# Kernel tuning notes

Measured on AMD Instinct MI355X. Metric: run time of the kernel, lower is better.

## Reference

```python
import jax, jax.numpy as jnp
import numpy as np

B = 524288
H = 64  # hidden_dim
D = 1   # input_dim


def setup_inputs() -> dict:
    key = jax.random.key(0)
    ks = jax.random.split(key, 16)
    s = 0.05
    inp = {
        "gradients": jax.random.normal(ks[0], (B, D), jnp.float32),
        "parameters": jax.random.normal(ks[1], (B, D), jnp.float32),
        "momentum": jax.random.normal(ks[2], (B, D), jnp.float32),
        "h0": jax.random.normal(ks[3], (B, H), jnp.float32),
        "c0": jax.random.normal(ks[4], (B, H), jnp.float32),
        # input_processor: Linear(3D->H), ReLU, Linear(H->H)
        "W1": jax.random.normal(ks[5], (H, 3 * D), jnp.float32) * s,
        "b1": jax.random.normal(ks[6], (H,), jnp.float32) * s,
        "W2": jax.random.normal(ks[7], (H, H), jnp.float32) * s,
        "b2": jax.random.normal(ks[8], (H,), jnp.float32) * s,
        # LSTM cell (PyTorch layout: gates stacked i,f,g,o -> 4H rows)
        "W_ih": jax.random.normal(ks[9], (4 * H, H), jnp.float32) * s,
        "W_hh": jax.random.normal(ks[10], (4 * H, H), jnp.float32) * s,
        "b_ih": jax.random.normal(ks[11], (4 * H,), jnp.float32) * s,
        "b_hh": jax.random.normal(ks[12], (4 * H,), jnp.float32) * s,
        # output_layer: Linear(H->D)
        "W_out": jax.random.normal(ks[13], (D, H), jnp.float32) * s,
        "b_out": jax.random.normal(ks[14], (D,), jnp.float32) * s,
    }
    return inp


def reference(gradients, parameters, momentum, h0, c0,
              W1, b1, W2, b2, W_ih, W_hh, b_ih, b_hh, W_out, b_out):
    # momentum update
    m = 0.9 * momentum + gradients                      # [B, D]
    feats = jnp.concatenate([gradients, parameters, m], axis=-1)  # [B, 3D]
    # small MLP
    x = jax.nn.relu(feats @ W1.T + b1) @ W2.T + b2      # [B, H]
    # single-step LSTM cell, PyTorch gate order i, f, g, o
    gates = x @ W_ih.T + b_ih + h0 @ W_hh.T + b_hh      # [B, 4H]
    i, f, g, o = jnp.split(gates, 4, axis=-1)
    c1 = jax.nn.sigmoid(f) * c0 + jax.nn.sigmoid(i) * jnp.tanh(g)
    h1 = jax.nn.sigmoid(o) * jnp.tanh(c1)               # [B, H]
    update = h1 @ W_out.T + b_out                       # [B, D]
    return update
```

## Files before the change

kernel.cpp:

```cpp
#include <hip/hip_runtime.h>
#include <hip/hip_bf16.h>
#include <stdint.h>


typedef __attribute__((ext_vector_type(8))) short   short8;
typedef __attribute__((ext_vector_type(8))) __bf16  bf16x8;
typedef __attribute__((ext_vector_type(4))) float   floatx4;

__device__ __forceinline__ unsigned short f2bf_bits(float x){
    unsigned u = __builtin_bit_cast(unsigned, x);
    u = u + 0x7fffu + ((u >> 16) & 1u);
    return (unsigned short)(u >> 16);
}
__device__ __forceinline__ float bf2f(unsigned short s){
    unsigned u = ((unsigned)s) << 16;
    return __builtin_bit_cast(float, u);
}
__device__ __forceinline__ float sigm(float x){ return 1.0f / (1.0f + __expf(-x)); }
__device__ __forceinline__ float tanh_fast(float x){ return 1.0f - 2.0f / (1.0f + __expf(2.0f*x)); }

__global__ __launch_bounds__(256) void prep_kernel(
    const float* __restrict__ W2, const float* __restrict__ b2,
    const float* __restrict__ W_ih, const float* __restrict__ W_hh,
    const float* __restrict__ b_ih, const float* __restrict__ b_hh,
    unsigned short* __restrict__ wc, float* __restrict__ biasc)
{
    __shared__ float W2s[64*64];
    __shared__ float b2s[64];
    __shared__ float wihs[16*64];
    const int tid = threadIdx.x;
    const int b   = blockIdx.x;

    for (int i = 0; i < 4; i++){
        int idx = i*1024 + tid*4;
        *(float4*)(W2s + idx) = *(const float4*)(W2 + idx);
    }
    if (tid < 64) b2s[tid] = b2[tid];
    {
        int idx = tid*4;
        *(float4*)(wihs + idx) = *(const float4*)(W_ih + b*16*64 + idx);
    }
    __syncthreads();

    const int nl = tid >> 4;
    const int n  = b*16 + nl;
    const int jg = tid & 15;
    const int j  = jg*4;
    const int T  = n >> 4;

    float a0=0.f, a1=0.f, a2=0.f, a3=0.f;
    for (int h = 0; h < 64; h++){
        float wv = wihs[nl*64 + h];
        const float* w2r = W2s + h*64 + j;
        a0 += wv*w2r[0]; a1 += wv*w2r[1]; a2 += wv*w2r[2]; a3 += wv*w2r[3];
    }
    auto store4 = [&](int k, float v0, float v1, float v2, float v3){
        int s    = k >> 5;
        int lane = ((k >> 3) & 3)*16 + (n & 15);
        int off  = (T*4 + s)*512 + lane*8 + (k & 7);
        ushort4 v; v.x=f2bf_bits(v0); v.y=f2bf_bits(v1); v.z=f2bf_bits(v2); v.w=f2bf_bits(v3);
        *(ushort4*)(wc + off) = v;
    };
    store4(j, a0, a1, a2, a3);
    {
        const float* src = W_hh + n*64 + j;
        store4(64 + j, src[0], src[1], src[2], src[3]);
    }
    if (jg == 0){
        float s = b_ih[n] + b_hh[n];
        for (int h = 0; h < 64; h++) s += wihs[nl*64 + h]*b2s[h];
        biasc[n] = s;
    }
}

__global__ __launch_bounds__(512, 4) void main_kernel(
    const float* __restrict__ grad, const float* __restrict__ param,
    const float* __restrict__ mom,  const float* __restrict__ h0,
    const float* __restrict__ c0,   const float* __restrict__ W1,
    const float* __restrict__ b1,   const float* __restrict__ Wout,
    const float* __restrict__ bout,
    const unsigned short* __restrict__ wc, const float* __restrict__ biasc,
    float* __restrict__ out)
{
    __shared__ unsigned short A_l[64*136];
    __shared__ unsigned short gates_l[4*64*68];
    __shared__ float psum_l[64*17];
    __shared__ float feats_l[3*64];
    __shared__ float w1_l[3*64];
    __shared__ float b1_l[64];
    __shared__ float wout_l[64];
    __shared__ float bias_l[256];

    const int tid  = threadIdx.x;
    const int lane = tid & 63;
    const int w    = tid >> 6;
    const long row0 = (long)blockIdx.x * 64;

    for (int it = 0; it < 2; it++){
        int flat = it*2048 + tid*4;
        int row = flat >> 6, col = flat & 63;
        float4 v = *(const float4*)(h0 + (row0 + row)*64 + col);
        ushort4 s; s.x=f2bf_bits(v.x); s.y=f2bf_bits(v.y); s.z=f2bf_bits(v.z); s.w=f2bf_bits(v.w);
        *(ushort4*)(A_l + row*136 + 64 + col) = s;
    }
    if (tid < 192)      w1_l[(tid % 3)*64 + tid/3] = W1[tid];
    else if (tid < 256) b1_l[tid - 192]  = b1[tid - 192];
    else if (tid < 320) wout_l[tid - 256] = Wout[tid - 256];
    else if (tid >= 448){
        int r = tid - 448;
        float g = grad[row0 + r], p = param[row0 + r], mo = mom[row0 + r];
        feats_l[r] = g; feats_l[64 + r] = p; feats_l[128 + r] = 0.9f*mo + g;
    }
    if (tid < 256) bias_l[tid] = biasc[tid];
    __syncthreads();

    {
        int row = tid & 63;
        int jb  = (tid >> 6) * 8;
        float g = feats_l[row], p = feats_l[64+row], m = feats_l[128+row];
        ushort4 sa, sb;
        unsigned short tv[8];
        #pragma unroll
        for (int jj = 0; jj < 8; jj++){
            int j = jb + jj;
            float v = w1_l[j]*g + w1_l[64+j]*p + w1_l[128+j]*m + b1_l[j];
            v = v > 0.f ? v : 0.f;
            tv[jj] = f2bf_bits(v);
        }
        sa.x=tv[0]; sa.y=tv[1]; sa.z=tv[2]; sa.w=tv[3];
        sb.x=tv[4]; sb.y=tv[5]; sb.z=tv[6]; sb.w=tv[7];
        *(ushort4*)(A_l + row*136 + jb)     = sa;
        *(ushort4*)(A_l + row*136 + jb + 4) = sb;
    }
    __syncthreads();

    const int l15 = lane & 15, q = lane >> 4;
    floatx4 acc[4][2];
    bf16x8  bfr[2][4];
    #pragma unroll
    for (int t = 0; t < 2; t++){
        int T = w*2 + t;
        float bv = bias_l[T*16 + l15];
        #pragma unroll
        for (int m = 0; m < 4; m++) acc[m][t] = (floatx4){bv, bv, bv, bv};
        #pragma unroll
        for (int s = 0; s < 4; s++)
            bfr[t][s] = __builtin_bit_cast(bf16x8,
                *(const short8*)(wc + (T*4 + s)*512 + lane*8));
    }
    #pragma unroll
    for (int m = 0; m < 4; m++){
        bf16x8 afr[4];
        const unsigned short* abase = A_l + (m*16 + l15)*136 + q*8;
        #pragma unroll
        for (int s = 0; s < 4; s++)
            afr[s] = __builtin_bit_cast(bf16x8, *(const short8*)(abase + s*32));
        #pragma unroll
        for (int t = 0; t < 2; t++)
            #pragma unroll
            for (int s = 0; s < 4; s++)
                acc[m][t] = __builtin_amdgcn_mfma_f32_16x16x32_bf16(
                                afr[s], bfr[t][s], acc[m][t], 0, 0, 0);
    }
    #pragma unroll
    for (int t = 0; t < 2; t++){
        int n = (w*2 + t)*16 + l15;
        int gg = n >> 6, j = n & 63;
        #pragma unroll
        for (int m = 0; m < 4; m++)
            #pragma unroll
            for (int r = 0; r < 4; r++){
                int row = m*16 + q*4 + r;
                gates_l[(gg*64 + row)*68 + j] = f2bf_bits(acc[m][t][r]);
            }
    }
    __syncthreads();

    for (int it = 0; it < 2; it++){
        int task = it*512 + tid;
        int row  = task >> 4;
        int j0   = (task & 15) * 4;
        float4 c0v = *(const float4*)(c0 + (row0 + row)*64 + j0);
        const unsigned short* gp = gates_l + row*68 + j0;
        ushort4 iv = *(const ushort4*)(gp + 0*64*68);
        ushort4 fv = *(const ushort4*)(gp + 1*64*68);
        ushort4 gv = *(const ushort4*)(gp + 2*64*68);
        ushort4 ov = *(const ushort4*)(gp + 3*64*68);
        float c0a[4] = {c0v.x, c0v.y, c0v.z, c0v.w};
        unsigned short ia[4] = {iv.x, iv.y, iv.z, iv.w};
        unsigned short fa[4] = {fv.x, fv.y, fv.z, fv.w};
        unsigned short ga[4] = {gv.x, gv.y, gv.z, gv.w};
        unsigned short oa[4] = {ov.x, ov.y, ov.z, ov.w};
        float part = 0.f;
        #pragma unroll
        for (int k = 0; k < 4; k++){
            float i_ = sigm(bf2f(ia[k]));
            float f_ = sigm(bf2f(fa[k]));
            float g_ = tanh_fast(bf2f(ga[k]));
            float o_ = sigm(bf2f(oa[k]));
            float c1 = f_*c0a[k] + i_*g_;
            float h1 = o_*tanh_fast(c1);
            part += h1 * wout_l[j0 + k];
        }
        psum_l[row*17 + (task & 15)] = part;
    }
    __syncthreads();

    if (tid < 64){
        float s = bout[0];
        #pragma unroll
        for (int k = 0; k < 16; k++) s += psum_l[tid*17 + k];
        out[row0 + tid] = s;
    }
}

extern "C" void kernel_launch(void* const* d_in, const int* in_sizes, int n_in,
                              void* d_out, int out_size, void* d_ws, size_t ws_size,
                              hipStream_t stream)
{
    const float* grad  = (const float*)d_in[0];
    const float* param = (const float*)d_in[1];
    const float* mom   = (const float*)d_in[2];
    const float* h0    = (const float*)d_in[3];
    const float* c0    = (const float*)d_in[4];
    const float* W1    = (const float*)d_in[5];
    const float* b1    = (const float*)d_in[6];
    const float* W2    = (const float*)d_in[7];
    const float* b2    = (const float*)d_in[8];
    const float* W_ih  = (const float*)d_in[9];
    const float* W_hh  = (const float*)d_in[10];
    const float* b_ih  = (const float*)d_in[11];
    const float* b_hh  = (const float*)d_in[12];
    const float* Wout  = (const float*)d_in[13];
    const float* bout  = (const float*)d_in[14];

    unsigned short* wc = (unsigned short*)d_ws;
    float* biasc       = (float*)((char*)d_ws + 65536);

    prep_kernel<<<16, 256, 0, stream>>>(W2, b2, W_ih, W_hh, b_ih, b_hh, wc, biasc);

    const int nblocks = 524288 / 64;
    main_kernel<<<nblocks, 512, 0, stream>>>(grad, param, mom, h0, c0,
                                             W1, b1, Wout, bout, wc, biasc,
                                             (float*)d_out);
}
```

Measured before the change: 362.8 us.

## Restructure LSTM kernel so each wave owns 16 rows with register-resident gates

Each wave now computes all 256 gate columns for its own 16 rows. The A fragments are built directly in registers from h0 and the MLP output, and the whole combined weight matrix is staged in LDS per block. Because the gate math, cell update and output dot product happen in registers with a shuffle reduction, the LDS round-trips for the A tile, the gates and the partial sums are gone, along with most barriers. Blocks cover 128 rows, and exp/rcp use hardware intrinsics. The costs are a 64KB LDS weight copy per block, which limits occupancy, uncoalesced strided c0 loads, and high register pressure from 16 accumulators.

```diff
diff --git a/kernel.cpp b/kernel.cpp
--- a/kernel.cpp
+++ b/kernel.cpp
@@ -3,7 +3,6 @@
 #include <stdint.h>
 
 
-typedef __attribute__((ext_vector_type(8))) short   short8;
 typedef __attribute__((ext_vector_type(8))) __bf16  bf16x8;
 typedef __attribute__((ext_vector_type(4))) float   floatx4;
 
@@ -12,12 +11,23 @@
     u = u + 0x7fffu + ((u >> 16) & 1u);
     return (unsigned short)(u >> 16);
 }
-__device__ __forceinline__ float bf2f(unsigned short s){
-    unsigned u = ((unsigned)s) << 16;
-    return __builtin_bit_cast(float, u);
-}
-__device__ __forceinline__ float sigm(float x){ return 1.0f / (1.0f + __expf(-x)); }
-__device__ __forceinline__ float tanh_fast(float x){ return 1.0f - 2.0f / (1.0f + __expf(2.0f*x)); }
+__device__ __forceinline__ unsigned pk2(float lo, float hi){
+    return ((unsigned)f2bf_bits(hi) << 16) | (unsigned)f2bf_bits(lo);
+}
+__device__ __forceinline__ bf16x8 pack8(float4 a, float4 b){
+    union { unsigned u[4]; bf16x8 v; } p;
+    p.u[0] = pk2(a.x, a.y); p.u[1] = pk2(a.z, a.w);
+    p.u[2] = pk2(b.x, b.y); p.u[3] = pk2(b.z, b.w);
+    return p.v;
+}
+__device__ __forceinline__ float sigm(float x){
+    float e = __builtin_amdgcn_exp2f(-1.442695041f * x);
+    return __builtin_amdgcn_rcpf(1.0f + e);
+}
+__device__ __forceinline__ float tanh_fast(float x){
+    float e = __builtin_amdgcn_exp2f(2.885390082f * x);
+    return 1.0f - 2.0f * __builtin_amdgcn_rcpf(1.0f + e);
+}
 
 __global__ __launch_bounds__(256) void prep_kernel(
     const float* __restrict__ W2, const float* __restrict__ b2,
@@ -82,135 +92,114 @@
     const unsigned short* __restrict__ wc, const float* __restrict__ biasc,
     float* __restrict__ out)
 {
-    __shared__ unsigned short A_l[64*136];
-    __shared__ unsigned short gates_l[4*64*68];
-    __shared__ float psum_l[64*17];
-    __shared__ float feats_l[3*64];
-    __shared__ float w1_l[3*64];
-    __shared__ float b1_l[64];
-    __shared__ float wout_l[64];
-    __shared__ float bias_l[256];
+    __shared__ __align__(16) unsigned short wc_l[32768];
+    __shared__ float  bias_l[256];
+    __shared__ float4 w1p_l[64];
 
     const int tid  = threadIdx.x;
     const int lane = tid & 63;
     const int w    = tid >> 6;
-    const long row0 = (long)blockIdx.x * 64;
-
-    for (int it = 0; it < 2; it++){
-        int flat = it*2048 + tid*4;
-        int row = flat >> 6, col = flat & 63;
-        float4 v = *(const float4*)(h0 + (row0 + row)*64 + col);
-        ushort4 s; s.x=f2bf_bits(v.x); s.y=f2bf_bits(v.y); s.z=f2bf_bits(v.z); s.w=f2bf_bits(v.w);
-        *(ushort4*)(A_l + row*136 + 64 + col) = s;
-    }
-    if (tid < 192)      w1_l[(tid % 3)*64 + tid/3] = W1[tid];
-    else if (tid < 256) b1_l[tid - 192]  = b1[tid - 192];
-    else if (tid < 320) wout_l[tid - 256] = Wout[tid - 256];
-    else if (tid >= 448){
-        int r = tid - 448;
-        float g = grad[row0 + r], p = param[row0 + r], mo = mom[row0 + r];
-        feats_l[r] = g; feats_l[64 + r] = p; feats_l[128 + r] = 0.9f*mo + g;
+    const int l15  = lane & 15;
+    const int q    = lane >> 4;
+    const long row0 = (long)blockIdx.x * 128;
+
+    {
+        const float4* src = (const float4*)wc;
+        float4*       dst = (float4*)wc_l;
+        #pragma unroll
+        for (int i = 0; i < 8; i++)
+            dst[i*512 + tid] = src[i*512 + tid];
     }
     if (tid < 256) bias_l[tid] = biasc[tid];
+    if (tid >= 256 && tid < 320){
+        int j = tid - 256;
+        w1p_l[j] = make_float4(W1[j*3], W1[j*3+1], W1[j*3+2], b1[j]);
+    }
+
+    const long rA = row0 + w*16 + l15;
+    float g = grad[rA], p = param[rA], mo = mom[rA];
+    float m = 0.9f*mo + g;
+
+    const float* hrow = h0 + rA*64;
+    float4 ha = *(const float4*)(hrow + q*8);
+    float4 hb = *(const float4*)(hrow + q*8 + 4);
+    float4 hc = *(const float4*)(hrow + 32 + q*8);
+    float4 hd = *(const float4*)(hrow + 32 + q*8 + 4);
+
     __syncthreads();
 
-    {
-        int row = tid & 63;
-        int jb  = (tid >> 6) * 8;
-        float g = feats_l[row], p = feats_l[64+row], m = feats_l[128+row];
-        ushort4 sa, sb;
-        unsigned short tv[8];
+    float rv[16];
+    #pragma unroll
+    for (int s = 0; s < 2; s++)
         #pragma unroll
         for (int jj = 0; jj < 8; jj++){
-            int j = jb + jj;
-            float v = w1_l[j]*g + w1_l[64+j]*p + w1_l[128+j]*m + b1_l[j];
-            v = v > 0.f ? v : 0.f;
-            tv[jj] = f2bf_bits(v);
+            int j = s*32 + q*8 + jj;
+            float4 wr = w1p_l[j];
+            float v = fmaf(wr.x, g, fmaf(wr.y, p, fmaf(wr.z, m, wr.w)));
+            rv[s*8+jj] = v > 0.f ? v : 0.f;
         }
-        sa.x=tv[0]; sa.y=tv[1]; sa.z=tv[2]; sa.w=tv[3];
-        sb.x=tv[4]; sb.y=tv[5]; sb.z=tv[6]; sb.w=tv[7];
-        *(ushort4*)(A_l + row*136 + jb)     = sa;
-        *(ushort4*)(A_l + row*136 + jb + 4) = sb;
-    }
-    __syncthreads();
-
-    const int l15 = lane & 15, q = lane >> 4;
-    floatx4 acc[4][2];
-    bf16x8  bfr[2][4];
-    #pragma unroll
-    for (int t = 0; t < 2; t++){
-        int T = w*2 + t;
+    bf16x8 afr[4];
+    afr[0] = pack8(make_float4(rv[0],rv[1],rv[2],rv[3]),
+                   make_float4(rv[4],rv[5],rv[6],rv[7]));
+    afr[1] = pack8(make_float4(rv[8],rv[9],rv[10],rv[11]),
+                   make_float4(rv[12],rv[13],rv[14],rv[15]));
+    afr[2] = pack8(ha, hb);
+    afr[3] = pack8(hc, hd);
+
+    floatx4 acc[16];
+    #pragma unroll
+    for (int T = 0; T < 16; T++){
         float bv = bias_l[T*16 + l15];
-        #pragma unroll
-        for (int m = 0; m < 4; m++) acc[m][t] = (floatx4){bv, bv, bv, bv};
-        #pragma unroll
-        for (int s = 0; s < 4; s++)
-            bfr[t][s] = __builtin_bit_cast(bf16x8,
-                *(const short8*)(wc + (T*4 + s)*512 + lane*8));
-    }
-    #pragma unroll
-    for (int m = 0; m < 4; m++){
-        bf16x8 afr[4];
-        const unsigned short* abase = A_l + (m*16 + l15)*136 + q*8;
-        #pragma unroll
-        for (int s = 0; s < 4; s++)
-            afr[s] = __builtin_bit_cast(bf16x8, *(const short8*)(abase + s*32));
-        #pragma unroll
-        for (int t = 0; t < 2; t++)
-            #pragma unroll
-            for (int s = 0; s < 4; s++)
-                acc[m][t] = __builtin_amdgcn_mfma_f32_16x16x32_bf16(
-                                afr[s], bfr[t][s], acc[m][t], 0, 0, 0);
-    }
-    #pragma unroll
-    for (int t = 0; t < 2; t++){
-        int n = (w*2 + t)*16 + l15;
-        int gg = n >> 6, j = n & 63;
-        #pragma unroll
-        for (int m = 0; m < 4; m++)
-            #pragma unroll
-            for (int r = 0; r < 4; r++){
-                int row = m*16 + q*4 + r;
-                gates_l[(gg*64 + row)*68 + j] = f2bf_bits(acc[m][t][r]);
-            }
-    }
-    __syncthreads();
-
-    for (int it = 0; it < 2; it++){
-        int task = it*512 + tid;
-        int row  = task >> 4;
-        int j0   = (task & 15) * 4;
-        float4 c0v = *(const float4*)(c0 + (row0 + row)*64 + j0);
-        const unsigned short* gp = gates_l + row*68 + j0;
-        ushort4 iv = *(const ushort4*)(gp + 0*64*68);
-        ushort4 fv = *(const ushort4*)(gp + 1*64*68);
-        ushort4 gv = *(const ushort4*)(gp + 2*64*68);
-        ushort4 ov = *(const ushort4*)(gp + 3*64*68);
-        float c0a[4] = {c0v.x, c0v.y, c0v.z, c0v.w};
-        unsigned short ia[4] = {iv.x, iv.y, iv.z, iv.w};
-        unsigned short fa[4] = {fv.x, fv.y, fv.z, fv.w};
-        unsigned short ga[4] = {gv.x, gv.y, gv.z, gv.w};
-        unsigned short oa[4] = {ov.x, ov.y, ov.z, ov.w};
-        float part = 0.f;
-        #pragma unroll
-        for (int k = 0; k < 4; k++){
-            float i_ = sigm(bf2f(ia[k]));
-            float f_ = sigm(bf2f(fa[k]));
-            float g_ = tanh_fast(bf2f(ga[k]));
-            float o_ = sigm(bf2f(oa[k]));
-            float c1 = f_*c0a[k] + i_*g_;
-            float h1 = o_*tanh_fast(c1);
-            part += h1 * wout_l[j0 + k];
+        const unsigned short* cb = wc_l + T*2048 + lane*8;
+        bf16x8 b0 = *(const bf16x8*)(cb);
+        bf16x8 b1f = *(const bf16x8*)(cb + 512);
+        bf16x8 b2f = *(const bf16x8*)(cb + 1024);
+        bf16x8 b3f = *(const bf16x8*)(cb + 1536);
+        acc[T] = __builtin_amdgcn_mfma_f32_16x16x32_bf16(afr[0], b0,
+                     (floatx4){bv, bv, bv, bv}, 0, 0, 0);
+        acc[T] = __builtin_amdgcn_mfma_f32_16x16x32_bf16(afr[1], b1f, acc[T], 0, 0, 0);
+        acc[T] = __builtin_amdgcn_mfma_f32_16x16x32_bf16(afr[2], b2f, acc[T], 0, 0, 0);
+        acc[T] = __builtin_amdgcn_mfma_f32_16x16x32_bf16(afr[3], b3f, acc[T], 0, 0, 0);
+    }
+
+    const float* c0base = c0 + (row0 + w*16 + q*4)*64 + l15;
+    float c0v[4][4];
+    #pragma unroll
+    for (int jh = 0; jh < 4; jh++)
+        #pragma unroll
+        for (int r = 0; r < 4; r++)
+            c0v[jh][r] = c0base[r*64 + jh*16];
+
+    float wo[4];
+    #pragma unroll
+    for (int jh = 0; jh < 4; jh++) wo[jh] = Wout[jh*16 + l15];
+    const float bout0 = bout[0];
+
+    float red[4] = {0.f, 0.f, 0.f, 0.f};
+    #pragma unroll
+    for (int jh = 0; jh < 4; jh++)
+        #pragma unroll
+        for (int r = 0; r < 4; r++){
+            float iv = sigm(acc[jh][r]);
+            float fv = sigm(acc[4+jh][r]);
+            float gv = tanh_fast(acc[8+jh][r]);
+            float ov = sigm(acc[12+jh][r]);
+            float c1 = fmaf(fv, c0v[jh][r], iv*gv);
+            float h1 = ov * tanh_fast(c1);
+            red[r] = fmaf(h1, wo[jh], red[r]);
         }
-        psum_l[row*17 + (task & 15)] = part;
-    }
-    __syncthreads();
-
-    if (tid < 64){
-        float s = bout[0];
-        #pragma unroll
-        for (int k = 0; k < 16; k++) s += psum_l[tid*17 + k];
-        out[row0 + tid] = s;
+
+    #pragma unroll
+    for (int mset = 1; mset < 16; mset <<= 1)
+        #pragma unroll
+        for (int r = 0; r < 4; r++)
+            red[r] += __shfl_xor(red[r], mset, 64);
+
+    if (l15 == 0){
+        long orow = row0 + w*16 + q*4;
+        #pragma unroll
+        for (int r = 0; r < 4; r++)
+            out[orow + r] = red[r] + bout0;
     }
 }
 
@@ -239,7 +228,7 @@
 
     prep_kernel<<<16, 256, 0, stream>>>(W2, b2, W_ih, W_hh, b_ih, b_hh, wc, biasc);
 
-    const int nblocks = 524288 / 64;
+    const int nblocks = 524288 / 128;
     main_kernel<<<nblocks, 512, 0, stream>>>(grad, param, mom, h0, c0,
                                              W1, b1, Wout, bout, wc, biasc,
                                              (float*)d_out);
```

After: 310.6 us. 1.17x faster.
